# Kernel tuning notes

Hardware: AMD Instinct MI355X
Metric: run time of the kernel (lower is better)

## Reference

```python
import jax, jax.numpy as jnp
import numpy as np

N_NODES = 50000
N_EDGES = 600000
D = 128  # in_channels == out_channels
LN_EPS = 1e-5


def _mlp(h, W1, b1, W2, b2, ln_g, ln_b):
    # anemoi MLP: Linear -> SiLU -> Linear -> LayerNorm
    h = jax.nn.silu(h @ W1 + b1)
    h = h @ W2 + b2
    mu = jnp.mean(h, axis=-1, keepdims=True)
    var = jnp.var(h, axis=-1, keepdims=True)
    return (h - mu) * jax.lax.rsqrt(var + LN_EPS) * ln_g + ln_b


def setup_inputs() -> dict:
    key = jax.random.key(0)
    ks = jax.random.split(key, 12)
    s = lambda fan_in: 1.0 / np.sqrt(fan_in)
    inp = {
        "x": jax.random.normal(ks[0], (N_NODES, D), dtype=jnp.float32),
        "edge_attr": jax.random.normal(ks[1], (N_EDGES, D), dtype=jnp.float32),
        "edge_index": jax.random.randint(ks[2], (2, N_EDGES), 0, N_NODES, dtype=jnp.int32),
        # conv edge-MLP params: in = 3*D (x_dst, x_src, edge_attr)
        "eW1": jax.random.uniform(ks[3], (3 * D, D), jnp.float32, -s(3 * D), s(3 * D)),
        "eb1": jnp.zeros((D,), jnp.float32),
        "eW2": jax.random.uniform(ks[4], (D, D), jnp.float32, -s(D), s(D)),
        "eb2": jnp.zeros((D,), jnp.float32),
        "eln_g": jnp.ones((D,), jnp.float32),
        "eln_b": jnp.zeros((D,), jnp.float32),
        # node MLP params: in = 2*D (x, aggregated messages)
        "nW1": jax.random.uniform(ks[5], (2 * D, D), jnp.float32, -s(2 * D), s(2 * D)),
        "nb1": jnp.zeros((D,), jnp.float32),
        "nW2": jax.random.uniform(ks[6], (D, D), jnp.float32, -s(D), s(D)),
        "nb2": jnp.zeros((D,), jnp.float32),
        "nln_g": jnp.ones((D,), jnp.float32),
        "nln_b": jnp.zeros((D,), jnp.float32),
    }
    return inp


def reference(x, edge_attr, edge_index,
              eW1, eb1, eW2, eb2, eln_g, eln_b,
              nW1, nb1, nW2, nb2, nln_g, nln_b):
    src = edge_index[0]  # j
    dst = edge_index[1]  # i
    # GraphConv.message: edge MLP over cat([x_i, x_j, edge_attr])
    edge_in = jnp.concatenate([x[dst], x[src], edge_attr], axis=1)  # [E, 3D]
    edges_new = _mlp(edge_in, eW1, eb1, eW2, eb2, eln_g, eln_b)      # [E, D]
    # aggregate: scatter-add to destination nodes (chunking sums to the same result)
    out = jax.ops.segment_sum(edges_new, dst, num_segments=x.shape[0])  # [N, D]
    # node update: concat + MLP + residual
    nodes_new = _mlp(jnp.concatenate([x, out], axis=1), nW1, nb1, nW2, nb2, nln_g, nln_b) + x
    return nodes_new, edges_new
```

## Files before the change

### kernel.cpp

```cpp
#include <hip/hip_runtime.h>

#define D       128
#define NNODES  50000
#define NEDGES  600000
#define TE      64
#define TN      64
#define BLK     256
#define LN_EPS  1e-5f

typedef float  fx4    __attribute__((ext_vector_type(4)));
typedef float  f32x4  __attribute__((ext_vector_type(4)));
typedef __bf16 bf16x4 __attribute__((ext_vector_type(4)));
typedef __bf16 bf16x8 __attribute__((ext_vector_type(8)));

#define EW1F_OFF 0
#define EW2F_OFF (128 * 384)
#define NW1F_OFF (EW2F_OFF + 128 * 128)
#define NW2F_OFF (NW1F_OFF + 128 * 256)
#define WS_ELEMS (NW2F_OFF + 128 * 128)

__device__ __forceinline__ float silu_f(float z) {
    return z * (1.0f / (1.0f + __expf(-z)));
}

__global__ __launch_bounds__(256) void prep_weights(
    const float* __restrict__ eW1, const float* __restrict__ eW2,
    const float* __restrict__ nW1, const float* __restrict__ nW2,
    __bf16* __restrict__ ws)
{
    int idx = blockIdx.x * 256 + threadIdx.x;
    if (idx >= WS_ELEMS) return;
    const float* src;
    int local;
    if (idx < EW2F_OFF)      { src = eW1; local = idx; }
    else if (idx < NW1F_OFF) { src = eW2; local = idx - EW2F_OFF; }
    else if (idx < NW2F_OFF) { src = nW1; local = idx - NW1F_OFF; }
    else                     { src = nW2; local = idx - NW2F_OFF; }
    const int f   = local >> 9;
    const int rem = local & 511;
    const int l   = rem >> 3;
    const int j   = rem & 7;
    const int ks  = f >> 3;
    const int nf  = f & 7;
    const int n   = (nf << 4) + (l & 15);
    const int k   = (ks << 5) + ((l >> 4) << 3) + j;
    ws[idx] = (__bf16)src[(size_t)k * D + n];
}

__global__ __launch_bounds__(BLK, 4) void edge_kernel(
    const float* __restrict__ x,
    const float* __restrict__ edge_attr,
    const int*   __restrict__ edge_index,
    const __bf16* __restrict__ W1f,
    const float* __restrict__ b1,
    const __bf16* __restrict__ W2f,
    const float* __restrict__ b2,
    const float* __restrict__ lng, const float* __restrict__ lnb,
    float* __restrict__ edges_out,
    float* __restrict__ agg)
{
    __shared__ __bf16 in_t[TE][264];
    __shared__ int    src_s[TE], dst_s[TE];

    const int tid = threadIdx.x;
    const int e0g = blockIdx.x * TE;

    if (tid < TE) {
        src_s[tid] = edge_index[e0g + tid];
        dst_s[tid] = edge_index[NEDGES + e0g + tid];
    }
    __syncthreads();

    const int lane  = tid & 63;
    const int wid   = tid >> 6;
    const int wrow0 = wid << 4;
    const int c16   = lane & 15;
    const int kq    = lane >> 4;
    const int ks8   = kq << 3;
    const int lo8   = lane << 3;

    bf16x8 aE[4];
    {
        const float* ep = edge_attr + (size_t)(e0g + wrow0 + c16) * D + ks8;
        #pragma unroll
        for (int ks2 = 0; ks2 < 4; ++ks2) {
            fx4 v0 = *(const fx4*)(ep + (ks2 << 5));
            fx4 v1 = *(const fx4*)(ep + (ks2 << 5) + 4);
            bf16x8 a;
            #pragma unroll
            for (int j = 0; j < 4; ++j) { a[j] = (__bf16)v0[j]; a[j + 4] = (__bf16)v1[j]; }
            aE[ks2] = a;
        }
    }

    #pragma unroll
    for (int it = 0; it < 8; ++it) {
        const int idx = tid + it * BLK;
        const int e   = idx >> 5;
        const int c4  = (idx & 31) << 2;
        fx4 v = *(const fx4*)&x[(size_t)dst_s[e] * D + c4];
        bf16x4 h;
        #pragma unroll
        for (int j = 0; j < 4; ++j) h[j] = (__bf16)v[j];
        *(bf16x4*)&in_t[e][c4] = h;
    }
    #pragma unroll
    for (int it = 0; it < 8; ++it) {
        const int idx = tid + it * BLK;
        const int e   = idx >> 5;
        const int c4  = (idx & 31) << 2;
        fx4 v = *(const fx4*)&x[(size_t)src_s[e] * D + c4];
        bf16x4 h;
        #pragma unroll
        for (int j = 0; j < 4; ++j) h[j] = (__bf16)v[j];
        *(bf16x4*)&in_t[e][128 + c4] = h;
    }
    __syncthreads();

    f32x4 acc[8];
    #pragma unroll
    for (int nf = 0; nf < 8; ++nf) acc[nf] = (f32x4){0.f, 0.f, 0.f, 0.f};

    #pragma unroll
    for (int ks = 0; ks < 12; ++ks) {
        bf16x8 a = (ks < 8) ? *(const bf16x8*)&in_t[wrow0 + c16][(ks << 5) + ks8]
                            : aE[ks - 8];
        const __bf16* wp = W1f + ((size_t)(ks << 3) << 9) + lo8;
        #pragma unroll
        for (int nf = 0; nf < 8; ++nf) {
            bf16x8 b = *(const bf16x8*)(wp + (nf << 9));
            acc[nf] = __builtin_amdgcn_mfma_f32_16x16x32_bf16(a, b, acc[nf], 0, 0, 0);
        }
    }

    #pragma unroll
    for (int nf = 0; nf < 8; ++nf) {
        const float bb = b1[nf * 16 + c16];
        #pragma unroll
        for (int r = 0; r < 4; ++r) {
            float h = silu_f(acc[nf][r] + bb);
            in_t[wrow0 + kq * 4 + r][nf * 16 + c16] = (__bf16)h;
        }
    }

    f32x4 acc2[8];
    #pragma unroll
    for (int nf = 0; nf < 8; ++nf) acc2[nf] = (f32x4){0.f, 0.f, 0.f, 0.f};

    #pragma unroll
    for (int ks = 0; ks < 4; ++ks) {
        bf16x8 a = *(const bf16x8*)&in_t[wrow0 + c16][(ks << 5) + ks8];
        const __bf16* wp = W2f + ((size_t)(ks << 3) << 9) + lo8;
        #pragma unroll
        for (int nf = 0; nf < 8; ++nf) {
            bf16x8 b = *(const bf16x8*)(wp + (nf << 9));
            acc2[nf] = __builtin_amdgcn_mfma_f32_16x16x32_bf16(a, b, acc2[nf], 0, 0, 0);
        }
    }

    float b2v[8], gv[8], bvv[8];
    #pragma unroll
    for (int nf = 0; nf < 8; ++nf) {
        b2v[nf] = b2[nf * 16 + c16];
        gv[nf]  = lng[nf * 16 + c16];
        bvv[nf] = lnb[nf * 16 + c16];
    }

    float s[4] = {0.f, 0.f, 0.f, 0.f}, q[4] = {0.f, 0.f, 0.f, 0.f};
    #pragma unroll
    for (int nf = 0; nf < 8; ++nf)
        #pragma unroll
        for (int r = 0; r < 4; ++r) {
            float zz = acc2[nf][r] + b2v[nf];
            acc2[nf][r] = zz;
            s[r] += zz;
            q[r] += zz * zz;
        }
    #pragma unroll
    for (int m = 1; m <= 8; m <<= 1)
        #pragma unroll
        for (int r = 0; r < 4; ++r) {
            s[r] += __shfl_xor(s[r], m, 64);
            q[r] += __shfl_xor(q[r], m, 64);
        }

    #pragma unroll
    for (int r = 0; r < 4; ++r) {
        const float mu   = s[r] * (1.0f / 128.0f);
        const float var  = q[r] * (1.0f / 128.0f) - mu * mu;
        const float rstd = rsqrtf(var + LN_EPS);
        const int row = wrow0 + kq * 4 + r;
        const size_t erow = (size_t)(e0g + row) * D;
        float* ap = agg + (size_t)dst_s[row] * D;
        #pragma unroll
        for (int nf = 0; nf < 8; ++nf) {
            const int col = nf * 16 + c16;
            float o = (acc2[nf][r] - mu) * rstd * gv[nf] + bvv[nf];
            edges_out[erow + col] = o;
            atomicAdd(ap + col, o);
        }
    }
}

__global__ __launch_bounds__(BLK, 4) void node_kernel(
    const float* __restrict__ x,
    const float* __restrict__ agg,
    const __bf16* __restrict__ W1f,
    const float* __restrict__ b1,
    const __bf16* __restrict__ W2f,
    const float* __restrict__ b2,
    const float* __restrict__ lng, const float* __restrict__ lnb,
    float* __restrict__ nodes_out)
{
    __shared__ __bf16 in_t[TN][264];

    const int tid = threadIdx.x;
    const int r0g = blockIdx.x * TN;

    #pragma unroll
    for (int it = 0; it < 8; ++it) {
        const int idx = tid + it * BLK;
        const int e   = idx >> 5;
        const int c4  = (idx & 31) << 2;
        const int row = r0g + e;
        fx4 v = {0.f, 0.f, 0.f, 0.f};
        if (row < NNODES) v = *(const fx4*)&x[(size_t)row * D + c4];
        bf16x4 h;
        #pragma unroll
        for (int j = 0; j < 4; ++j) h[j] = (__bf16)v[j];
        *(bf16x4*)&in_t[e][c4] = h;
    }
    #pragma unroll
    for (int it = 0; it < 8; ++it) {
        const int idx = tid + it * BLK;
        const int e   = idx >> 5;
        const int c4  = (idx & 31) << 2;
        const int row = r0g + e;
        fx4 v = {0.f, 0.f, 0.f, 0.f};
        if (row < NNODES) v = *(const fx4*)&agg[(size_t)row * D + c4];
        bf16x4 h;
        #pragma unroll
        for (int j = 0; j < 4; ++j) h[j] = (__bf16)v[j];
        *(bf16x4*)&in_t[e][128 + c4] = h;
    }
    __syncthreads();

    const int lane  = tid & 63;
    const int wid   = tid >> 6;
    const int wrow0 = wid << 4;
    const int c16   = lane & 15;
    const int kq    = lane >> 4;
    const int ks8   = kq << 3;
    const int lo8   = lane << 3;

    f32x4 acc[8];
    #pragma unroll
    for (int nf = 0; nf < 8; ++nf) acc[nf] = (f32x4){0.f, 0.f, 0.f, 0.f};

    #pragma unroll
    for (int ks = 0; ks < 8; ++ks) {
        bf16x8 a = *(const bf16x8*)&in_t[wrow0 + c16][(ks << 5) + ks8];
        const __bf16* wp = W1f + ((size_t)(ks << 3) << 9) + lo8;
        #pragma unroll
        for (int nf = 0; nf < 8; ++nf) {
            bf16x8 b = *(const bf16x8*)(wp + (nf << 9));
            acc[nf] = __builtin_amdgcn_mfma_f32_16x16x32_bf16(a, b, acc[nf], 0, 0, 0);
        }
    }

    #pragma unroll
    for (int nf = 0; nf < 8; ++nf) {
        const float bb = b1[nf * 16 + c16];
        #pragma unroll
        for (int r = 0; r < 4; ++r) {
            float h = silu_f(acc[nf][r] + bb);
            in_t[wrow0 + kq * 4 + r][nf * 16 + c16] = (__bf16)h;
        }
    }

    f32x4 acc2[8];
    #pragma unroll
    for (int nf = 0; nf < 8; ++nf) acc2[nf] = (f32x4){0.f, 0.f, 0.f, 0.f};

    #pragma unroll
    for (int ks = 0; ks < 4; ++ks) {
        bf16x8 a = *(const bf16x8*)&in_t[wrow0 + c16][(ks << 5) + ks8];
        const __bf16* wp = W2f + ((size_t)(ks << 3) << 9) + lo8;
        #pragma unroll
        for (int nf = 0; nf < 8; ++nf) {
            bf16x8 b = *(const bf16x8*)(wp + (nf << 9));
            acc2[nf] = __builtin_amdgcn_mfma_f32_16x16x32_bf16(a, b, acc2[nf], 0, 0, 0);
        }
    }

    float b2v[8], gv[8], bvv[8];
    #pragma unroll
    for (int nf = 0; nf < 8; ++nf) {
        b2v[nf] = b2[nf * 16 + c16];
        gv[nf]  = lng[nf * 16 + c16];
        bvv[nf] = lnb[nf * 16 + c16];
    }

    float s[4] = {0.f, 0.f, 0.f, 0.f}, q[4] = {0.f, 0.f, 0.f, 0.f};
    #pragma unroll
    for (int nf = 0; nf < 8; ++nf)
        #pragma unroll
        for (int r = 0; r < 4; ++r) {
            float zz = acc2[nf][r] + b2v[nf];
            acc2[nf][r] = zz;
            s[r] += zz;
            q[r] += zz * zz;
        }
    #pragma unroll
    for (int m = 1; m <= 8; m <<= 1)
        #pragma unroll
        for (int r = 0; r < 4; ++r) {
            s[r] += __shfl_xor(s[r], m, 64);
            q[r] += __shfl_xor(q[r], m, 64);
        }

    #pragma unroll
    for (int r = 0; r < 4; ++r) {
        const float mu   = s[r] * (1.0f / 128.0f);
        const float var  = q[r] * (1.0f / 128.0f) - mu * mu;
        const float rstd = rsqrtf(var + LN_EPS);
        const int row = r0g + wrow0 + kq * 4 + r;
        if (row >= NNODES) continue;
        const size_t orow = (size_t)row * D;
        #pragma unroll
        for (int nf = 0; nf < 8; ++nf) {
            const int col = nf * 16 + c16;
            float o = (acc2[nf][r] - mu) * rstd * gv[nf] + bvv[nf] + x[orow + col];
            nodes_out[orow + col] = o;
        }
    }
}

extern "C" void kernel_launch(void* const* d_in, const int* in_sizes, int n_in,
                              void* d_out, int out_size, void* d_ws, size_t ws_size,
                              hipStream_t stream) {
    (void)in_sizes; (void)n_in; (void)ws_size; (void)out_size;

    const float* x         = (const float*)d_in[0];
    const float* edge_attr = (const float*)d_in[1];
    const int*   edge_idx  = (const int*)  d_in[2];
    const float* eW1 = (const float*)d_in[3];
    const float* eb1 = (const float*)d_in[4];
    const float* eW2 = (const float*)d_in[5];
    const float* eb2 = (const float*)d_in[6];
    const float* elg = (const float*)d_in[7];
    const float* elb = (const float*)d_in[8];
    const float* nW1 = (const float*)d_in[9];
    const float* nb1 = (const float*)d_in[10];
    const float* nW2 = (const float*)d_in[11];
    const float* nb2 = (const float*)d_in[12];
    const float* nlg = (const float*)d_in[13];
    const float* nlb = (const float*)d_in[14];

    float* out       = (float*)d_out;
    float* nodes_out = out;
    float* edges_out = out + (size_t)NNODES * D;

    __bf16* ws = (__bf16*)d_ws;

    prep_weights<<<(WS_ELEMS + 255) / 256, 256, 0, stream>>>(eW1, eW2, nW1, nW2, ws);

    hipMemsetAsync(nodes_out, 0, (size_t)NNODES * D * sizeof(float), stream);

    edge_kernel<<<NEDGES / TE, BLK, 0, stream>>>(
        x, edge_attr, edge_idx,
        ws + EW1F_OFF, eb1, ws + EW2F_OFF, eb2, elg, elb,
        edges_out, nodes_out);

    node_kernel<<<(NNODES + TN - 1) / TN, BLK, 0, stream>>>(
        x, nodes_out,
        ws + NW1F_OFF, nb1, ws + NW2F_OFF, nb2, nlg, nlb,
        nodes_out);
}
```

Before: 445.0 us.

## Precompute per-node first-layer projections to cut per-edge GEMM work

Splits the edge MLP's first linear layer by linearity: x_dst@W1a + b1 and x_src@W1b are computed once per node into workspace buffers, and each edge then gathers and adds the two projected rows instead of multiplying a 384-wide concatenated input. This removes two thirds of the first-layer MFMA work per edge (600k edges against 50k nodes). The cost is an extra node kernel, about 51 MB of fp32 workspace, fp32 gathers of projected rows in place of raw x, and a bf16 rounding of the summed partials. The original kernel is kept as a fallback when the workspace is too small.

```diff
diff --git a/kernel.cpp b/kernel.cpp
--- a/kernel.cpp
+++ b/kernel.cpp
@@ -18,6 +18,10 @@
 #define NW1F_OFF (EW2F_OFF + 128 * 128)
 #define NW2F_OFF (NW1F_OFF + 128 * 256)
 #define WS_ELEMS (NW2F_OFF + 128 * 128)
+#define W_BYTES  (WS_ELEMS * 2)
+#define PD_OFF      ((size_t)W_BYTES)
+#define PS_OFF      (PD_OFF + (size_t)NNODES * D * 4)
+#define WS_NEED_PRE (PS_OFF + (size_t)NNODES * D * 4)
 
 __device__ __forceinline__ float silu_f(float z) {
     return z * (1.0f / (1.0f + __expf(-z)));
@@ -47,7 +51,214 @@
     ws[idx] = (__bf16)src[(size_t)k * D + n];
 }
 
-__global__ __launch_bounds__(BLK, 4) void edge_kernel(
+__global__ __launch_bounds__(256) void pre_nodes(
+    const float* __restrict__ x,
+    const __bf16* __restrict__ W1f,
+    const float* __restrict__ b1,
+    float* __restrict__ Pd,
+    float* __restrict__ Ps)
+{
+    __shared__ __bf16 xt[TN][136];
+
+    const int tid = threadIdx.x;
+    const int r0g = blockIdx.x * TN;
+    const int lane  = tid & 63;
+    const int wid   = tid >> 6;
+    const int wrow0 = wid << 4;
+    const int c16   = lane & 15;
+    const int kq    = lane >> 4;
+    const int ks8   = kq << 3;
+    const int lo8   = lane << 3;
+
+    #pragma unroll
+    for (int pass = 0; pass < 8; ++pass) {
+        const int row = wrow0 + (pass << 1) + (lane >> 5);
+        const int gr  = r0g + row;
+        const int c4  = (lane & 31) << 2;
+        fx4 v = {0.f, 0.f, 0.f, 0.f};
+        if (gr < NNODES) v = *(const fx4*)&x[(size_t)gr * D + c4];
+        bf16x4 h;
+        #pragma unroll
+        for (int j = 0; j < 4; ++j) h[j] = (__bf16)v[j];
+        *(bf16x4*)&xt[row][c4] = h;
+    }
+
+    f32x4 acc_d[8], acc_s[8];
+    #pragma unroll
+    for (int nf = 0; nf < 8; ++nf) {
+        acc_d[nf] = (f32x4){0.f, 0.f, 0.f, 0.f};
+        acc_s[nf] = (f32x4){0.f, 0.f, 0.f, 0.f};
+    }
+
+    #pragma unroll
+    for (int ks = 0; ks < 4; ++ks) {
+        bf16x8 a = *(const bf16x8*)&xt[wrow0 + c16][(ks << 5) + ks8];
+        const __bf16* wpd = W1f + ((size_t)(ks << 3) << 9) + lo8;
+        const __bf16* wps = W1f + ((size_t)((4 + ks) << 3) << 9) + lo8;
+        #pragma unroll
+        for (int nf = 0; nf < 8; ++nf) {
+            bf16x8 bd = *(const bf16x8*)(wpd + (nf << 9));
+            bf16x8 bs = *(const bf16x8*)(wps + (nf << 9));
+            acc_d[nf] = __builtin_amdgcn_mfma_f32_16x16x32_bf16(a, bd, acc_d[nf], 0, 0, 0);
+            acc_s[nf] = __builtin_amdgcn_mfma_f32_16x16x32_bf16(a, bs, acc_s[nf], 0, 0, 0);
+        }
+    }
+
+    #pragma unroll
+    for (int nf = 0; nf < 8; ++nf) {
+        const int col = nf * 16 + c16;
+        const float bb = b1[col];
+        #pragma unroll
+        for (int r = 0; r < 4; ++r) {
+            const int row = r0g + wrow0 + kq * 4 + r;
+            if (row < NNODES) {
+                Pd[(size_t)row * D + col] = acc_d[nf][r] + bb;
+                Ps[(size_t)row * D + col] = acc_s[nf][r];
+            }
+        }
+    }
+}
+
+__global__ __launch_bounds__(BLK, 5) void edge_kernel_pre(
+    const float* __restrict__ edge_attr,
+    const int*   __restrict__ edge_index,
+    const float* __restrict__ Pd,
+    const float* __restrict__ Ps,
+    const __bf16* __restrict__ W1f,
+    const __bf16* __restrict__ W2f,
+    const float* __restrict__ b2,
+    const float* __restrict__ lng, const float* __restrict__ lnb,
+    float* __restrict__ edges_out,
+    float* __restrict__ agg)
+{
+    __shared__ __bf16 sum_t[TE][136];
+
+    const int tid = threadIdx.x;
+    const int e0g = blockIdx.x * TE;
+    const int lane  = tid & 63;
+    const int wid   = tid >> 6;
+    const int wrow0 = wid << 4;
+    const int c16   = lane & 15;
+    const int kq    = lane >> 4;
+    const int ks8   = kq << 3;
+    const int lo8   = lane << 3;
+
+    #pragma unroll
+    for (int pass = 0; pass < 8; ++pass) {
+        const int row = wrow0 + (pass << 1) + (lane >> 5);
+        const int ge  = e0g + row;
+        const int dn  = edge_index[NEDGES + ge];
+        const int sn  = edge_index[ge];
+        const int c4  = (lane & 31) << 2;
+        fx4 a = *(const fx4*)&Pd[(size_t)dn * D + c4];
+        fx4 b = *(const fx4*)&Ps[(size_t)sn * D + c4];
+        bf16x4 h;
+        #pragma unroll
+        for (int j = 0; j < 4; ++j) h[j] = (__bf16)(a[j] + b[j]);
+        *(bf16x4*)&sum_t[row][c4] = h;
+    }
+
+    bf16x8 aE[4];
+    {
+        const float* ep = edge_attr + (size_t)(e0g + wrow0 + c16) * D + ks8;
+        #pragma unroll
+        for (int ks2 = 0; ks2 < 4; ++ks2) {
+            fx4 v0 = *(const fx4*)(ep + (ks2 << 5));
+            fx4 v1 = *(const fx4*)(ep + (ks2 << 5) + 4);
+            bf16x8 a;
+            #pragma unroll
+            for (int j = 0; j < 4; ++j) { a[j] = (__bf16)v0[j]; a[j + 4] = (__bf16)v1[j]; }
+            aE[ks2] = a;
+        }
+    }
+
+    f32x4 acc[8];
+    #pragma unroll
+    for (int nf = 0; nf < 8; ++nf) acc[nf] = (f32x4){0.f, 0.f, 0.f, 0.f};
+
+    #pragma unroll
+    for (int ks2 = 0; ks2 < 4; ++ks2) {
+        const __bf16* wp = W1f + ((size_t)((8 + ks2) << 3) << 9) + lo8;
+        #pragma unroll
+        for (int nf = 0; nf < 8; ++nf) {
+            bf16x8 b = *(const bf16x8*)(wp + (nf << 9));
+            acc[nf] = __builtin_amdgcn_mfma_f32_16x16x32_bf16(aE[ks2], b, acc[nf], 0, 0, 0);
+        }
+    }
+
+    #pragma unroll
+    for (int nf = 0; nf < 8; ++nf) {
+        #pragma unroll
+        for (int r = 0; r < 4; ++r) {
+            const int row = wrow0 + kq * 4 + r;
+            const int col = nf * 16 + c16;
+            float z = acc[nf][r] + (float)sum_t[row][col];
+            sum_t[row][col] = (__bf16)silu_f(z);
+        }
+    }
+
+    f32x4 acc2[8];
+    #pragma unroll
+    for (int nf = 0; nf < 8; ++nf) acc2[nf] = (f32x4){0.f, 0.f, 0.f, 0.f};
+
+    #pragma unroll
+    for (int ks = 0; ks < 4; ++ks) {
+        bf16x8 a = *(const bf16x8*)&sum_t[wrow0 + c16][(ks << 5) + ks8];
+        const __bf16* wp = W2f + ((size_t)(ks << 3) << 9) + lo8;
+        #pragma unroll
+        for (int nf = 0; nf < 8; ++nf) {
+            bf16x8 b = *(const bf16x8*)(wp + (nf << 9));
+            acc2[nf] = __builtin_amdgcn_mfma_f32_16x16x32_bf16(a, b, acc2[nf], 0, 0, 0);
+        }
+    }
+
+    float b2v[8], gv[8], bvv[8];
+    #pragma unroll
+    for (int nf = 0; nf < 8; ++nf) {
+        b2v[nf] = b2[nf * 16 + c16];
+        gv[nf]  = lng[nf * 16 + c16];
+        bvv[nf] = lnb[nf * 16 + c16];
+    }
+
+    float s[4] = {0.f, 0.f, 0.f, 0.f}, q[4] = {0.f, 0.f, 0.f, 0.f};
+    #pragma unroll
+    for (int nf = 0; nf < 8; ++nf)
+        #pragma unroll
+        for (int r = 0; r < 4; ++r) {
+            float zz = acc2[nf][r] + b2v[nf];
+            acc2[nf][r] = zz;
+            s[r] += zz;
+            q[r] += zz * zz;
+        }
+    #pragma unroll
+    for (int m = 1; m <= 8; m <<= 1)
+        #pragma unroll
+        for (int r = 0; r < 4; ++r) {
+            s[r] += __shfl_xor(s[r], m, 64);
+            q[r] += __shfl_xor(q[r], m, 64);
+        }
+
+    #pragma unroll
+    for (int r = 0; r < 4; ++r) {
+        const float mu   = s[r] * (1.0f / 128.0f);
+        const float var  = q[r] * (1.0f / 128.0f) - mu * mu;
+        const float rstd = rsqrtf(var + LN_EPS);
+        const int row = wrow0 + kq * 4 + r;
+        const int ge  = e0g + row;
+        const int dn  = edge_index[NEDGES + ge];
+        const size_t erow = (size_t)ge * D;
+        float* ap = agg + (size_t)dn * D;
+        #pragma unroll
+        for (int nf = 0; nf < 8; ++nf) {
+            const int col = nf * 16 + c16;
+            float o = (acc2[nf][r] - mu) * rstd * gv[nf] + bvv[nf];
+            edges_out[erow + col] = o;
+            atomicAdd(ap + col, o);
+        }
+    }
+}
+
+__global__ __launch_bounds__(BLK, 4) void edge_kernel_fb(
     const float* __restrict__ x,
     const float* __restrict__ edge_attr,
     const int*   __restrict__ edge_index,
@@ -339,7 +550,7 @@
 extern "C" void kernel_launch(void* const* d_in, const int* in_sizes, int n_in,
                               void* d_out, int out_size, void* d_ws, size_t ws_size,
                               hipStream_t stream) {
-    (void)in_sizes; (void)n_in; (void)ws_size; (void)out_size;
+    (void)in_sizes; (void)n_in; (void)out_size;
 
     const float* x         = (const float*)d_in[0];
     const float* edge_attr = (const float*)d_in[1];
@@ -361,16 +572,30 @@
     float* nodes_out = out;
     float* edges_out = out + (size_t)NNODES * D;
 
-    __bf16* ws = (__bf16*)d_ws;
+    char*   wsb = (char*)d_ws;
+    __bf16* ws  = (__bf16*)d_ws;
 
     prep_weights<<<(WS_ELEMS + 255) / 256, 256, 0, stream>>>(eW1, eW2, nW1, nW2, ws);
 
     hipMemsetAsync(nodes_out, 0, (size_t)NNODES * D * sizeof(float), stream);
 
-    edge_kernel<<<NEDGES / TE, BLK, 0, stream>>>(
-        x, edge_attr, edge_idx,
-        ws + EW1F_OFF, eb1, ws + EW2F_OFF, eb2, elg, elb,
-        edges_out, nodes_out);
+    if (ws_size >= WS_NEED_PRE) {
+        float* Pd = (float*)(wsb + PD_OFF);
+        float* Ps = (float*)(wsb + PS_OFF);
+
+        pre_nodes<<<(NNODES + TN - 1) / TN, BLK, 0, stream>>>(
+            x, ws + EW1F_OFF, eb1, Pd, Ps);
+
+        edge_kernel_pre<<<NEDGES / TE, BLK, 0, stream>>>(
+            edge_attr, edge_idx, Pd, Ps,
+            ws + EW1F_OFF, ws + EW2F_OFF, eb2, elg, elb,
+            edges_out, nodes_out);
+    } else {
+        edge_kernel_fb<<<NEDGES / TE, BLK, 0, stream>>>(
+            x, edge_attr, edge_idx,
+            ws + EW1F_OFF, eb1, ws + EW2F_OFF, eb2, elg, elb,
+            edges_out, nodes_out);
+    }
 
     node_kernel<<<(NNODES + TN - 1) / TN, BLK, 0, stream>>>(
         x, nodes_out,
```

Result: slower. 520.9 us (+17.1%).

## Make edge kernel persistent with register-resident weight slices per wave

Applied to the files above, without the earlier changes.

The edge MLP kernel becomes a persistent grid of 512 blocks that loop over 64-edge tiles. Each wave now owns a 32-column slice of the output and keeps its slice of both weight matrices in registers for the whole kernel, instead of rereading every weight fragment from global memory for each tile. Because each wave only sees part of the row, LayerNorm statistics are combined across waves through shared memory, which adds extra barriers. Register pressure rises (launch bounds drop to 2 blocks per SIMD), and there is no overlap of gather loads with compute between tiles, so latency hiding may suffer.

```diff
diff --git a/kernel.cpp b/kernel.cpp
--- a/kernel.cpp
+++ b/kernel.cpp
@@ -3,7 +3,7 @@
 #define D       128
 #define NNODES  50000
 #define NEDGES  600000
-#define TE      64
+#define NTILES  (NEDGES / 64)
 #define TN      64
 #define BLK     256
 #define LN_EPS  1e-5f
@@ -47,7 +47,7 @@
     ws[idx] = (__bf16)src[(size_t)k * D + n];
 }
 
-__global__ __launch_bounds__(BLK, 4) void edge_kernel(
+__global__ __launch_bounds__(BLK, 2) void edge_kernel_pw(
     const float* __restrict__ x,
     const float* __restrict__ edge_attr,
     const int*   __restrict__ edge_index,
@@ -59,145 +59,184 @@
     float* __restrict__ edges_out,
     float* __restrict__ agg)
 {
-    __shared__ __bf16 in_t[TE][264];
-    __shared__ int    src_s[TE], dst_s[TE];
-
-    const int tid = threadIdx.x;
-    const int e0g = blockIdx.x * TE;
-
-    if (tid < TE) {
-        src_s[tid] = edge_index[e0g + tid];
-        dst_s[tid] = edge_index[NEDGES + e0g + tid];
-    }
-    __syncthreads();
-
-    const int lane  = tid & 63;
-    const int wid   = tid >> 6;
-    const int wrow0 = wid << 4;
-    const int c16   = lane & 15;
-    const int kq    = lane >> 4;
-    const int ks8   = kq << 3;
-    const int lo8   = lane << 3;
-
-    bf16x8 aE[4];
-    {
-        const float* ep = edge_attr + (size_t)(e0g + wrow0 + c16) * D + ks8;
-        #pragma unroll
-        for (int ks2 = 0; ks2 < 4; ++ks2) {
-            fx4 v0 = *(const fx4*)(ep + (ks2 << 5));
-            fx4 v1 = *(const fx4*)(ep + (ks2 << 5) + 4);
-            bf16x8 a;
-            #pragma unroll
-            for (int j = 0; j < 4; ++j) { a[j] = (__bf16)v0[j]; a[j + 4] = (__bf16)v1[j]; }
-            aE[ks2] = a;
-        }
-    }
-
-    #pragma unroll
-    for (int it = 0; it < 8; ++it) {
-        const int idx = tid + it * BLK;
-        const int e   = idx >> 5;
-        const int c4  = (idx & 31) << 2;
-        fx4 v = *(const fx4*)&x[(size_t)dst_s[e] * D + c4];
-        bf16x4 h;
-        #pragma unroll
-        for (int j = 0; j < 4; ++j) h[j] = (__bf16)v[j];
-        *(bf16x4*)&in_t[e][c4] = h;
-    }
-    #pragma unroll
-    for (int it = 0; it < 8; ++it) {
-        const int idx = tid + it * BLK;
-        const int e   = idx >> 5;
-        const int c4  = (idx & 31) << 2;
-        fx4 v = *(const fx4*)&x[(size_t)src_s[e] * D + c4];
-        bf16x4 h;
-        #pragma unroll
-        for (int j = 0; j < 4; ++j) h[j] = (__bf16)v[j];
-        *(bf16x4*)&in_t[e][128 + c4] = h;
-    }
-    __syncthreads();
-
-    f32x4 acc[8];
-    #pragma unroll
-    for (int nf = 0; nf < 8; ++nf) acc[nf] = (f32x4){0.f, 0.f, 0.f, 0.f};
-
-    #pragma unroll
-    for (int ks = 0; ks < 12; ++ks) {
-        bf16x8 a = (ks < 8) ? *(const bf16x8*)&in_t[wrow0 + c16][(ks << 5) + ks8]
-                            : aE[ks - 8];
-        const __bf16* wp = W1f + ((size_t)(ks << 3) << 9) + lo8;
-        #pragma unroll
-        for (int nf = 0; nf < 8; ++nf) {
-            bf16x8 b = *(const bf16x8*)(wp + (nf << 9));
-            acc[nf] = __builtin_amdgcn_mfma_f32_16x16x32_bf16(a, b, acc[nf], 0, 0, 0);
-        }
-    }
-
-    #pragma unroll
-    for (int nf = 0; nf < 8; ++nf) {
-        const float bb = b1[nf * 16 + c16];
-        #pragma unroll
-        for (int r = 0; r < 4; ++r) {
-            float h = silu_f(acc[nf][r] + bb);
-            in_t[wrow0 + kq * 4 + r][nf * 16 + c16] = (__bf16)h;
-        }
-    }
-
-    f32x4 acc2[8];
-    #pragma unroll
-    for (int nf = 0; nf < 8; ++nf) acc2[nf] = (f32x4){0.f, 0.f, 0.f, 0.f};
-
-    #pragma unroll
-    for (int ks = 0; ks < 4; ++ks) {
-        bf16x8 a = *(const bf16x8*)&in_t[wrow0 + c16][(ks << 5) + ks8];
-        const __bf16* wp = W2f + ((size_t)(ks << 3) << 9) + lo8;
-        #pragma unroll
-        for (int nf = 0; nf < 8; ++nf) {
-            bf16x8 b = *(const bf16x8*)(wp + (nf << 9));
-            acc2[nf] = __builtin_amdgcn_mfma_f32_16x16x32_bf16(a, b, acc2[nf], 0, 0, 0);
-        }
-    }
-
-    float b2v[8], gv[8], bvv[8];
-    #pragma unroll
-    for (int nf = 0; nf < 8; ++nf) {
-        b2v[nf] = b2[nf * 16 + c16];
-        gv[nf]  = lng[nf * 16 + c16];
-        bvv[nf] = lnb[nf * 16 + c16];
-    }
-
-    float s[4] = {0.f, 0.f, 0.f, 0.f}, q[4] = {0.f, 0.f, 0.f, 0.f};
-    #pragma unroll
-    for (int nf = 0; nf < 8; ++nf)
-        #pragma unroll
-        for (int r = 0; r < 4; ++r) {
-            float zz = acc2[nf][r] + b2v[nf];
-            acc2[nf][r] = zz;
-            s[r] += zz;
-            q[r] += zz * zz;
-        }
-    #pragma unroll
-    for (int m = 1; m <= 8; m <<= 1)
-        #pragma unroll
-        for (int r = 0; r < 4; ++r) {
-            s[r] += __shfl_xor(s[r], m, 64);
-            q[r] += __shfl_xor(q[r], m, 64);
-        }
-
-    #pragma unroll
-    for (int r = 0; r < 4; ++r) {
-        const float mu   = s[r] * (1.0f / 128.0f);
-        const float var  = q[r] * (1.0f / 128.0f) - mu * mu;
-        const float rstd = rsqrtf(var + LN_EPS);
-        const int row = wrow0 + kq * 4 + r;
-        const size_t erow = (size_t)(e0g + row) * D;
-        float* ap = agg + (size_t)dst_s[row] * D;
-        #pragma unroll
-        for (int nf = 0; nf < 8; ++nf) {
-            const int col = nf * 16 + c16;
-            float o = (acc2[nf][r] - mu) * rstd * gv[nf] + bvv[nf];
-            edges_out[erow + col] = o;
-            atomicAdd(ap + col, o);
+    __shared__ __bf16 in_t[64][392];
+    __shared__ __bf16 h1_t[64][136];
+    __shared__ float  pr[64][12];
+
+    const int tid  = threadIdx.x;
+    const int lane = tid & 63;
+    const int w    = tid >> 6;
+    const int c16  = lane & 15;
+    const int kq   = lane >> 4;
+    const int ks8  = kq << 3;
+    const int lo8  = lane << 3;
+
+    bf16x8 W1r[12][2], W2r[4][2];
+    #pragma unroll
+    for (int ks = 0; ks < 12; ++ks)
+        #pragma unroll
+        for (int j = 0; j < 2; ++j)
+            W1r[ks][j] = *(const bf16x8*)&W1f[((size_t)(ks * 8 + 2 * w + j) << 9) + lo8];
+    #pragma unroll
+    for (int ks = 0; ks < 4; ++ks)
+        #pragma unroll
+        for (int j = 0; j < 2; ++j)
+            W2r[ks][j] = *(const bf16x8*)&W2f[((size_t)(ks * 8 + 2 * w + j) << 9) + lo8];
+
+    float b1v[2], b2v[2], gv[2], bvv[2];
+    #pragma unroll
+    for (int j = 0; j < 2; ++j) {
+        const int col = (2 * w + j) * 16 + c16;
+        b1v[j] = b1[col];
+        b2v[j] = b2[col];
+        gv[j]  = lng[col];
+        bvv[j] = lnb[col];
+    }
+
+    for (int t = blockIdx.x; t < NTILES; t += gridDim.x) {
+        const int e0g = t << 6;
+
+        #pragma unroll
+        for (int it = 0; it < 8; ++it) {
+            const int idx = tid + (it << 8);
+            const int e   = idx >> 5;
+            const int c4  = (idx & 31) << 2;
+            const int dn  = edge_index[NEDGES + e0g + e];
+            fx4 v = *(const fx4*)&x[(size_t)dn * D + c4];
+            bf16x4 h;
+            #pragma unroll
+            for (int j = 0; j < 4; ++j) h[j] = (__bf16)v[j];
+            *(bf16x4*)&in_t[e][c4] = h;
+        }
+        #pragma unroll
+        for (int it = 0; it < 8; ++it) {
+            const int idx = tid + (it << 8);
+            const int e   = idx >> 5;
+            const int c4  = (idx & 31) << 2;
+            const int sn  = edge_index[e0g + e];
+            fx4 v = *(const fx4*)&x[(size_t)sn * D + c4];
+            bf16x4 h;
+            #pragma unroll
+            for (int j = 0; j < 4; ++j) h[j] = (__bf16)v[j];
+            *(bf16x4*)&in_t[e][128 + c4] = h;
+        }
+        #pragma unroll
+        for (int it = 0; it < 8; ++it) {
+            const int idx = tid + (it << 8);
+            const int e   = idx >> 5;
+            const int c4  = (idx & 31) << 2;
+            fx4 v = *(const fx4*)&edge_attr[(size_t)(e0g + e) * D + c4];
+            bf16x4 h;
+            #pragma unroll
+            for (int j = 0; j < 4; ++j) h[j] = (__bf16)v[j];
+            *(bf16x4*)&in_t[e][256 + c4] = h;
+        }
+        __syncthreads();
+
+        f32x4 acc[4][2];
+        #pragma unroll
+        for (int mi = 0; mi < 4; ++mi)
+            #pragma unroll
+            for (int j = 0; j < 2; ++j) acc[mi][j] = (f32x4){0.f, 0.f, 0.f, 0.f};
+
+        #pragma unroll
+        for (int ks = 0; ks < 12; ++ks) {
+            bf16x8 a[4];
+            #pragma unroll
+            for (int mi = 0; mi < 4; ++mi)
+                a[mi] = *(const bf16x8*)&in_t[mi * 16 + c16][(ks << 5) + ks8];
+            #pragma unroll
+            for (int mi = 0; mi < 4; ++mi)
+                #pragma unroll
+                for (int j = 0; j < 2; ++j)
+                    acc[mi][j] = __builtin_amdgcn_mfma_f32_16x16x32_bf16(
+                        a[mi], W1r[ks][j], acc[mi][j], 0, 0, 0);
+        }
+
+        #pragma unroll
+        for (int mi = 0; mi < 4; ++mi)
+            #pragma unroll
+            for (int j = 0; j < 2; ++j) {
+                const int col = (2 * w + j) * 16 + c16;
+                #pragma unroll
+                for (int r = 0; r < 4; ++r)
+                    h1_t[mi * 16 + kq * 4 + r][col] =
+                        (__bf16)silu_f(acc[mi][j][r] + b1v[j]);
+            }
+        __syncthreads();
+
+        #pragma unroll
+        for (int mi = 0; mi < 4; ++mi)
+            #pragma unroll
+            for (int j = 0; j < 2; ++j) acc[mi][j] = (f32x4){0.f, 0.f, 0.f, 0.f};
+
+        #pragma unroll
+        for (int ks = 0; ks < 4; ++ks) {
+            bf16x8 a[4];
+            #pragma unroll
+            for (int mi = 0; mi < 4; ++mi)
+                a[mi] = *(const bf16x8*)&h1_t[mi * 16 + c16][(ks << 5) + ks8];
+            #pragma unroll
+            for (int mi = 0; mi < 4; ++mi)
+                #pragma unroll
+                for (int j = 0; j < 2; ++j)
+                    acc[mi][j] = __builtin_amdgcn_mfma_f32_16x16x32_bf16(
+                        a[mi], W2r[ks][j], acc[mi][j], 0, 0, 0);
+        }
+
+        #pragma unroll
+        for (int mi = 0; mi < 4; ++mi) {
+            float sl[4], ql[4];
+            #pragma unroll
+            for (int r = 0; r < 4; ++r) {
+                float z0 = acc[mi][0][r] + b2v[0];
+                float z1 = acc[mi][1][r] + b2v[1];
+                acc[mi][0][r] = z0;
+                acc[mi][1][r] = z1;
+                sl[r] = z0 + z1;
+                ql[r] = z0 * z0 + z1 * z1;
+            }
+            #pragma unroll
+            for (int m = 1; m <= 8; m <<= 1)
+                #pragma unroll
+                for (int r = 0; r < 4; ++r) {
+                    sl[r] += __shfl_xor(sl[r], m, 64);
+                    ql[r] += __shfl_xor(ql[r], m, 64);
+                }
+            if (c16 == 0) {
+                #pragma unroll
+                for (int r = 0; r < 4; ++r) {
+                    const int row = mi * 16 + kq * 4 + r;
+                    pr[row][2 * w]     = sl[r];
+                    pr[row][2 * w + 1] = ql[r];
+                }
+            }
+        }
+        __syncthreads();
+
+        #pragma unroll
+        for (int mi = 0; mi < 4; ++mi) {
+            #pragma unroll
+            for (int r = 0; r < 4; ++r) {
+                const int row = mi * 16 + kq * 4 + r;
+                f32x4 p0 = *(const f32x4*)&pr[row][0];
+                f32x4 p1 = *(const f32x4*)&pr[row][4];
+                const float s = p0[0] + p0[2] + p1[0] + p1[2];
+                const float q = p0[1] + p0[3] + p1[1] + p1[3];
+                const float mu   = s * (1.0f / 128.0f);
+                const float var  = q * (1.0f / 128.0f) - mu * mu;
+                const float rstd = rsqrtf(var + LN_EPS);
+                const int dn = edge_index[NEDGES + e0g + row];
+                const size_t erow = (size_t)(e0g + row) * D;
+                float* ap = agg + (size_t)dn * D;
+                #pragma unroll
+                for (int j = 0; j < 2; ++j) {
+                    const int col = (2 * w + j) * 16 + c16;
+                    float o = (acc[mi][j][r] - mu) * rstd * gv[j] + bvv[j];
+                    edges_out[erow + col] = o;
+                    atomicAdd(ap + col, o);
+                }
+            }
         }
     }
 }
@@ -367,7 +406,7 @@
 
     hipMemsetAsync(nodes_out, 0, (size_t)NNODES * D * sizeof(float), stream);
 
-    edge_kernel<<<NEDGES / TE, BLK, 0, stream>>>(
+    edge_kernel_pw<<<512, BLK, 0, stream>>>(
         x, edge_attr, edge_idx,
         ws + EW1F_OFF, eb1, ws + EW2F_OFF, eb2, elg, elb,
         edges_out, nodes_out);
```

Result: slower. 548.4 us (+23.2%).
